# Optimization experiments

Hardware: AMD Instinct MI355X
Metric: run time of the kernel (lower is better)

## Reference

```python
import jax, jax.numpy as jnp
import numpy as np

N_NODES = 100000
N_EDGES = 400000
N_GRAPHS = 5000
F_IN = 64
H = 128
OUT = 1
N_LAYERS = 3  # gat_conv + 2 atom_gats
NEG_SLOPE = 0.01


def _gat_conv(x_src, x_dst, src, dst, W, a_src, a_dst, b, num_dst):
    """PyG GATConv, heads=1, add_self_loops=False, negative_slope=0.01.

    x_src: [Ns, Fin], x_dst: [Nd, Fin]; src/dst: [E] int; W: [Fin, H];
    a_src, a_dst, b: [H]. Returns [Nd, H].
    """
    hs = x_src @ W                      # [Ns, H]
    hd = x_dst @ W                      # [Nd, H]
    as_n = hs @ a_src                   # [Ns]
    ad_n = hd @ a_dst                   # [Nd]
    e = jax.nn.leaky_relu(as_n[src] + ad_n[dst], NEG_SLOPE)  # [E]
    # segment softmax over destination nodes
    seg_max = jax.ops.segment_max(e, dst, num_segments=num_dst)
    seg_max = jnp.where(jnp.isfinite(seg_max), seg_max, 0.0)
    ex = jnp.exp(e - seg_max[dst])
    denom = jax.ops.segment_sum(ex, dst, num_segments=num_dst) + 1e-16
    alpha = ex / denom[dst]             # [E]
    out = jax.ops.segment_sum(alpha[:, None] * hs[src], dst, num_segments=num_dst)
    return out + b


def setup_inputs() -> dict:
    key = jax.random.key(0)
    ks = jax.random.split(key, 16)
    x = jax.random.normal(ks[0], (N_NODES, F_IN), dtype=jnp.float32)
    edge_index = jax.random.randint(ks[1], (2, N_EDGES), 0, N_NODES, dtype=jnp.int64)
    batch = jnp.sort(jax.random.randint(ks[2], (N_NODES,), 0, N_GRAPHS, dtype=jnp.int64))
    s_in = 1.0 / np.sqrt(F_IN)
    s_h = 1.0 / np.sqrt(H)
    W1 = jax.random.uniform(ks[3], (F_IN, H), jnp.float32, -s_in, s_in)
    b1 = jax.random.uniform(ks[4], (H,), jnp.float32, -s_in, s_in)
    gW = jax.random.normal(ks[5], (N_LAYERS, H, H), jnp.float32) * s_h
    g_asrc = jax.random.normal(ks[6], (N_LAYERS, H), jnp.float32) * s_h
    g_adst = jax.random.normal(ks[7], (N_LAYERS, H), jnp.float32) * s_h
    g_b = jnp.zeros((N_LAYERS, H), jnp.float32)
    mW = jax.random.normal(ks[8], (H, H), jnp.float32) * s_h
    m_asrc = jax.random.normal(ks[9], (H,), jnp.float32) * s_h
    m_adst = jax.random.normal(ks[10], (H,), jnp.float32) * s_h
    m_b = jnp.zeros((H,), jnp.float32)
    W2 = jax.random.uniform(ks[11], (H, OUT), jnp.float32, -s_h, s_h)
    b2 = jax.random.uniform(ks[12], (OUT,), jnp.float32, -s_h, s_h)
    return {"x": x, "edge_index": edge_index, "batch": batch,
            "W1": W1, "b1": b1, "gW": gW, "g_asrc": g_asrc,
            "g_adst": g_adst, "g_b": g_b, "mW": mW, "m_asrc": m_asrc,
            "m_adst": m_adst, "m_b": m_b, "W2": W2, "b2": b2}


def reference(x, edge_index, batch, W1, b1, gW, g_asrc, g_adst, g_b,
              mW, m_asrc, m_adst, m_b, W2, b2):
    src, dst = edge_index[0], edge_index[1]
    h = jax.nn.leaky_relu(x @ W1 + b1, NEG_SLOPE)            # lin1 + leaky_relu_
    for i in range(N_LAYERS):                                 # gat_conv + atom_gats
        h = jax.nn.elu(_gat_conv(h, h, src, dst, gW[i], g_asrc[i],
                                 g_adst[i], g_b[i], N_NODES))
    # global readout: node -> graph bipartite GAT
    pooled = jax.nn.relu(jax.ops.segment_sum(h, batch, num_segments=N_GRAPHS))
    row = jnp.arange(N_NODES)
    out = jax.nn.elu(_gat_conv(h, pooled, row, batch, mW, m_asrc,
                               m_adst, m_b, N_GRAPHS))
    return out @ W2 + b2                                      # [N_GRAPHS, OUT]
```

## Files before the change

### kernel.cpp

```cpp
#include <hip/hip_runtime.h>
#include <hip/hip_fp16.h>
#include <math.h>
#include <stdint.h>

#define DEV __device__ __forceinline__

using f32x4 = __attribute__((ext_vector_type(4))) float;
using half8 = __attribute__((ext_vector_type(8))) _Float16;
typedef union { uint4 u; half8 h; } u4h8;

DEV float lrelu(float x){ return x > 0.f ? x : 0.01f*x; }
DEV float elu1(float x){ return x > 0.f ? x : __expf(x)-1.f; }

DEV int lower_bound_i(const int* __restrict__ a, int n, int key){
  int lo = 0, hi = n;
  while (lo < hi){ int mid = (lo+hi)>>1; if (a[mid] < key) lo = mid+1; else hi = mid; }
  return lo;
}

__global__ void wprep(const float* __restrict__ W, unsigned short* __restrict__ Hi,
                      unsigned short* __restrict__ Lo, int K, int tot){
  int idx = blockIdx.x*256 + threadIdx.x;
  if (idx >= tot) return;
  int kn = K*128;
  int mat = idx / kn;
  int rem = idx - mat*kn;
  int k = rem >> 7;
  int n = rem & 127;
  float v = W[idx];
  __half h = __float2half_rn(v);
  float lo = (v - __half2float(h)) * 1024.f;
  size_t o = (size_t)mat*kn + (size_t)n*K + k;
  Hi[o] = __half_as_ushort(h);
  Lo[o] = __half_as_ushort(__float2half_rn(lo));
}

__global__ __launch_bounds__(256, 3) void gemm_lin1(
    const float* __restrict__ X, const unsigned short* __restrict__ Wt_hi,
    const unsigned short* __restrict__ Wt_lo, const float* __restrict__ bias,
    unsigned short* __restrict__ Ch, int M)
{
  const int tid = threadIdx.x;
  const int lane = tid & 63;
  const int wv = tid >> 6;
  const int ml = lane & 15;
  const int kg = lane >> 4;
  const int R0 = blockIdx.x * 64;

  __shared__ uint32_t sA[2][1024];
  __shared__ float sC[4][32][36];

  const unsigned short* bhp[2];
  const unsigned short* blp[2];
  #pragma unroll
  for (int nt = 0; nt < 2; ++nt){
    int n = wv*32 + nt*16 + ml;
    bhp[nt] = Wt_hi + (size_t)n*64 + kg*8;
    blp[nt] = Wt_lo + (size_t)n*64 + kg*8;
  }

  {
    int row = tid >> 2, kq = tid & 3;
    int gr = R0 + row; gr = gr < M ? gr : M-1;
    const float4* xp = (const float4*)(X + (size_t)gr*64 + kq*16);
    int sub = kq >> 1;
    #pragma unroll
    for (int i = 0; i < 4; ++i){
      float4 v = xp[i];
      __half2 h0 = __floats2half2_rn(v.x, v.y);
      __half2 h1 = __floats2half2_rn(v.z, v.w);
      int slot = (kq & 1)*2 + (i >> 1);
      int slot_s = slot ^ ((row >> 1) & 3);
      int byte = row*64 + slot_s*16 + (i & 1)*8;
      *(uint2*)((char*)&sA[sub][0] + byte) = make_uint2(*(uint32_t*)&h0, *(uint32_t*)&h1);
    }
  }
  __syncthreads();

  f32x4 accH[4][2], accL[4][2];
  #pragma unroll
  for (int mt = 0; mt < 4; ++mt)
    #pragma unroll
    for (int nt = 0; nt < 2; ++nt){
      accH[mt][nt] = (f32x4){0.f,0.f,0.f,0.f};
      accL[mt][nt] = (f32x4){0.f,0.f,0.f,0.f};
    }

  #pragma unroll
  for (int sc = 0; sc < 2; ++sc){
    u4h8 bh[2], bl[2];
    #pragma unroll
    for (int nt = 0; nt < 2; ++nt){
      bh[nt].u = *(const uint4*)(bhp[nt] + sc*32);
      bl[nt].u = *(const uint4*)(blp[nt] + sc*32);
    }
    const char* buf = (const char*)&sA[sc][0];
    #pragma unroll
    for (int mt = 0; mt < 4; ++mt){
      int row = mt*16 + ml;
      int ba = row*64 + ((kg ^ ((row >> 1) & 3)) * 16);
      u4h8 A_;
      A_.u = *(const uint4*)(buf + ba);
      #pragma unroll
      for (int nt = 0; nt < 2; ++nt){
        accH[mt][nt] = __builtin_amdgcn_mfma_f32_16x16x32_f16(A_.h, bh[nt].h, accH[mt][nt], 0, 0, 0);
        accL[mt][nt] = __builtin_amdgcn_mfma_f32_16x16x32_f16(A_.h, bl[nt].h, accL[mt][nt], 0, 0, 0);
      }
    }
  }

  float bv[2] = { bias[wv*32 + ml], bias[wv*32 + 16 + ml] };
  #pragma unroll
  for (int p = 0; p < 2; ++p){
    #pragma unroll
    for (int mh = 0; mh < 2; ++mh){
      int mt = p*2 + mh;
      #pragma unroll
      for (int nt = 0; nt < 2; ++nt){
        #pragma unroll
        for (int r = 0; r < 4; ++r){
          float v = accH[mt][nt][r] + accL[mt][nt][r] * 9.765625e-4f;
          v = lrelu(v + bv[nt]);
          sC[wv][mh*16 + kg*4 + r][nt*16 + ml] = v;
        }
      }
    }
    __syncthreads();
    #pragma unroll
    for (int j = 0; j < 4; ++j){
      int row_l = j*8 + (lane >> 3);
      int c4 = (lane & 7) * 4;
      int grow = R0 + p*32 + row_l;
      if (grow < M){
        float4 v = *(const float4*)&sC[wv][row_l][c4];
        int gcol = wv*32 + c4;
        __half2 h0 = __floats2half2_rn(v.x, v.y);
        __half2 h1 = __floats2half2_rn(v.z, v.w);
        *(uint2*)(Ch + (size_t)grow*128 + gcol) = make_uint2(*(uint32_t*)&h0, *(uint32_t*)&h1);
      }
    }
    __syncthreads();
  }
}

template<int OUTMODE, bool DOTA, bool DOTB>
__global__ __launch_bounds__(256, 3) void gemm_mfma(
    const unsigned short* __restrict__ Ah, const unsigned short* __restrict__ Wt_hi,
    const unsigned short* __restrict__ Wt_lo,
    const float* __restrict__ va, const float* __restrict__ vb,
    unsigned short* __restrict__ Ch,
    float* __restrict__ outa, float* __restrict__ outb, int M)
{
  constexpr int K = 128;
  const int tid = threadIdx.x;
  const int lane = tid & 63;
  const int wv = tid >> 6;
  const int ml = lane & 15;
  const int kg = lane >> 4;
  const int R0 = blockIdx.x * 64;

  __shared__ uint32_t sA[4][1024];
  __shared__ float sC[4][32][36];
  __shared__ float sd[4][64][2];

  const unsigned short* bhp[2];
  const unsigned short* blp[2];
  #pragma unroll
  for (int nt = 0; nt < 2; ++nt){
    int n = wv*32 + nt*16 + ml;
    bhp[nt] = Wt_hi + (size_t)n*K + kg*8;
    blp[nt] = Wt_lo + (size_t)n*K + kg*8;
  }

  auto STAGE = [&](int ch){
    #pragma unroll
    for (int j = 0; j < 2; ++j){
      int sc = ch*2 + j;
      int o = tid*16;
      int row = o >> 6;
      int t = (o >> 4) & 3;
      int gr = R0 + row; gr = gr < M ? gr : M-1;
      int jj = t ^ ((row >> 1) & 3);
      const char* src = (const char*)(Ah + (size_t)gr*K + sc*32 + jj*8);
      char* dst = (char*)(&sA[(ch & 1)*2 + j][0]) + wv*1024;
      __builtin_amdgcn_global_load_lds(
          (const __attribute__((address_space(1))) void*)src,
          (__attribute__((address_space(3))) void*)dst, 16, 0, 0);
    }
  };

  f32x4 accH[4][2], accL[4][2];
  #pragma unroll
  for (int mt = 0; mt < 4; ++mt)
    #pragma unroll
    for (int nt = 0; nt < 2; ++nt){
      accH[mt][nt] = (f32x4){0.f,0.f,0.f,0.f};
      accL[mt][nt] = (f32x4){0.f,0.f,0.f,0.f};
    }

  STAGE(0);
  u4h8 bh[2][2], bl[2][2];
  #pragma unroll
  for (int j = 0; j < 2; ++j)
    #pragma unroll
    for (int nt = 0; nt < 2; ++nt){
      bh[j][nt].u = *(const uint4*)(bhp[nt] + j*32);
      bl[j][nt].u = *(const uint4*)(blp[nt] + j*32);
    }
  __syncthreads();

  #pragma unroll
  for (int ch = 0; ch < 2; ++ch){
    u4h8 bhN[2][2], blN[2][2];
    if (ch == 0){
      STAGE(1);
      #pragma unroll
      for (int j = 0; j < 2; ++j)
        #pragma unroll
        for (int nt = 0; nt < 2; ++nt){
          bhN[j][nt].u = *(const uint4*)(bhp[nt] + (2 + j)*32);
          blN[j][nt].u = *(const uint4*)(blp[nt] + (2 + j)*32);
        }
    }
    #pragma unroll
    for (int js = 0; js < 2; ++js){
      const char* buf = (const char*)&sA[(ch & 1)*2 + js][0];
      #pragma unroll
      for (int mt = 0; mt < 4; ++mt){
        int row = mt*16 + ml;
        int ba = row*64 + ((kg ^ ((row >> 1) & 3)) * 16);
        u4h8 A_;
        A_.u = *(const uint4*)(buf + ba);
        #pragma unroll
        for (int nt = 0; nt < 2; ++nt){
          accH[mt][nt] = __builtin_amdgcn_mfma_f32_16x16x32_f16(A_.h, bh[js][nt].h, accH[mt][nt], 0, 0, 0);
          accL[mt][nt] = __builtin_amdgcn_mfma_f32_16x16x32_f16(A_.h, bl[js][nt].h, accL[mt][nt], 0, 0, 0);
        }
      }
    }
    __syncthreads();
    if (ch == 0){
      #pragma unroll
      for (int j = 0; j < 2; ++j)
        #pragma unroll
        for (int nt = 0; nt < 2; ++nt){ bh[j][nt] = bhN[j][nt]; bl[j][nt] = blN[j][nt]; }
    }
  }

  #pragma unroll
  for (int mt = 0; mt < 4; ++mt)
    #pragma unroll
    for (int nt = 0; nt < 2; ++nt)
      accH[mt][nt] = accH[mt][nt] + accL[mt][nt] * 9.765625e-4f;

  if constexpr (DOTA || DOTB){
    float vaL[2] = {0.f,0.f}, vbL[2] = {0.f,0.f};
    if constexpr (DOTA){ vaL[0] = va[wv*32 + ml]; vaL[1] = va[wv*32 + 16 + ml]; }
    if constexpr (DOTB){ vbL[0] = vb[wv*32 + ml]; vbL[1] = vb[wv*32 + 16 + ml]; }
    #pragma unroll
    for (int mt = 0; mt < 4; ++mt){
      #pragma unroll
      for (int r = 0; r < 4; ++r){
        float pa = 0.f, pb = 0.f;
        #pragma unroll
        for (int nt = 0; nt < 2; ++nt){
          float v = accH[mt][nt][r];
          if constexpr (DOTA) pa = fmaf(v, vaL[nt], pa);
          if constexpr (DOTB) pb = fmaf(v, vbL[nt], pb);
        }
        #pragma unroll
        for (int o = 8; o; o >>= 1){
          if constexpr (DOTA) pa += __shfl_xor(pa, o, 64);
          if constexpr (DOTB) pb += __shfl_xor(pb, o, 64);
        }
        if (ml == 0){
          int rl = mt*16 + kg*4 + r;
          sd[wv][rl][0] = pa;
          sd[wv][rl][1] = pb;
        }
      }
    }
    __syncthreads();
    if (tid < 64){
      int row = R0 + tid;
      if (row < M){
        if constexpr (DOTA)
          outa[row] = sd[0][tid][0] + sd[1][tid][0] + sd[2][tid][0] + sd[3][tid][0];
        if constexpr (DOTB)
          outb[row] = sd[0][tid][1] + sd[1][tid][1] + sd[2][tid][1] + sd[3][tid][1];
      }
    }
  }

  if constexpr (OUTMODE == 2){
    if constexpr (DOTA || DOTB) __syncthreads();
    #pragma unroll
    for (int p = 0; p < 2; ++p){
      #pragma unroll
      for (int mh = 0; mh < 2; ++mh){
        int mt = p*2 + mh;
        #pragma unroll
        for (int nt = 0; nt < 2; ++nt){
          #pragma unroll
          for (int r = 0; r < 4; ++r)
            sC[wv][mh*16 + kg*4 + r][nt*16 + ml] = accH[mt][nt][r];
        }
      }
      __syncthreads();
      #pragma unroll
      for (int j = 0; j < 4; ++j){
        int row_l = j*8 + (lane >> 3);
        int c4 = (lane & 7) * 4;
        int grow = R0 + p*32 + row_l;
        if (grow < M){
          float4 v = *(const float4*)&sC[wv][row_l][c4];
          int gcol = wv*32 + c4;
          __half2 h0 = __floats2half2_rn(v.x, v.y);
          __half2 h1 = __floats2half2_rn(v.z, v.w);
          *(uint2*)(Ch + (size_t)grow*128 + gcol) = make_uint2(*(uint32_t*)&h0, *(uint32_t*)&h1);
        }
      }
      __syncthreads();
    }
  }
}

__global__ void hist_k(const int* __restrict__ dstv, int* __restrict__ deg, int E){
  int e = blockIdx.x*256 + threadIdx.x;
  if (e < E) atomicAdd(&deg[dstv[e]], 1);
}

__global__ void scan_sum(const int* __restrict__ deg, int* __restrict__ bsum, int n){
  __shared__ int s4[4];
  int i = blockIdx.x*256 + threadIdx.x;
  int v = (i < n) ? deg[i] : 0;
  #pragma unroll
  for (int o = 32; o; o >>= 1) v += __shfl_down(v, o, 64);
  if ((threadIdx.x & 63) == 0) s4[threadIdx.x >> 6] = v;
  __syncthreads();
  if (threadIdx.x == 0) bsum[blockIdx.x] = s4[0]+s4[1]+s4[2]+s4[3];
}

__global__ void scan_blocksums(int* __restrict__ bsum, int nb){
  __shared__ int s[512];
  int t = threadIdx.x;
  s[t] = (t < nb) ? bsum[t] : 0;
  __syncthreads();
  for (int o = 1; o < 512; o <<= 1){
    int v = s[t];
    int u = (t >= o) ? s[t-o] : 0;
    __syncthreads();
    s[t] = v + u;
    __syncthreads();
  }
  if (t < nb) bsum[t] = t ? s[t-1] : 0;
}

__global__ void scan_final(const int* __restrict__ deg, const int* __restrict__ boff,
    int* __restrict__ rp, int* __restrict__ cur, int n, int E)
{
  __shared__ int wsum[4];
  int i = blockIdx.x*256 + threadIdx.x;
  int lane = threadIdx.x & 63, wv = threadIdx.x >> 6;
  int v = (i < n) ? deg[i] : 0;
  int inc = v;
  #pragma unroll
  for (int o = 1; o < 64; o <<= 1){
    int u = __shfl_up(inc, o, 64);
    if (lane >= o) inc += u;
  }
  if (lane == 63) wsum[wv] = inc;
  __syncthreads();
  int woff = boff[blockIdx.x];
  for (int wq = 0; wq < wv; ++wq) woff += wsum[wq];
  int excl = woff + inc - v;
  if (i < n){ rp[i] = excl; cur[i] = excl; }
  if (blockIdx.x == 0 && threadIdx.x == 0) rp[n] = E;
}

__global__ void scatter_k(const int* __restrict__ srcv, const int* __restrict__ dstv,
                          int* __restrict__ cur, int* __restrict__ ssorted, int E){
  int e = blockIdx.x*256 + threadIdx.x;
  if (e < E){
    int p = atomicAdd(&cur[dstv[e]], 1);
    ssorted[p] = srcv[e];
  }
}

DEV void gstep(const __half2* __restrict__ hs16, int lane, float alpha, int sid, int i,
               float& a0, float& a1){
  float al = __uint_as_float(__builtin_amdgcn_readlane(__float_as_uint(alpha), i));
  int sd = __builtin_amdgcn_readlane(sid, i);
  float2 f = __half22float2(hs16[(size_t)sd*64 + lane]);
  a0 = fmaf(al, f.x, a0);
  a1 = fmaf(al, f.y, a1);
}

__global__ __launch_bounds__(256) void gat_agg(const int* __restrict__ ssorted,
    const int* __restrict__ rp,
    const float* __restrict__ asn, const float* __restrict__ adn,
    const __half2* __restrict__ hs16, const float* __restrict__ bias,
    __half2* __restrict__ outp, int Nn)
{
  const int lane = threadIdx.x & 63;
  const int wv = threadIdx.x >> 6;
  const int d = blockIdx.x*4 + wv;
  if (d >= Nn) return;
  const int lo = rp[d], hi = rp[d+1];
  const int deg = hi - lo;
  float acc0 = 0.f, acc1 = 0.f;
  if (deg > 0){
    const float ad = adn[d];
    if (deg <= 64){
      int sid = 0; float lg = -1e30f;
      if (lane < deg){
        sid = ssorted[lo + lane];
        lg = lrelu(asn[sid] + ad);
      }
      float m = lg;
      if (deg <= 8){
        if (deg > 4) m = fmaxf(m, __shfl_xor(m, 4, 64));
        m = fmaxf(m, __shfl_xor(m, 2, 64));
        m = fmaxf(m, __shfl_xor(m, 1, 64));
        float p = (lane < deg) ? __expf(lg - m) : 0.f;
        float s = p;
        if (deg > 4) s += __shfl_xor(s, 4, 64);
        s += __shfl_xor(s, 2, 64);
        s += __shfl_xor(s, 1, 64);
        float alpha = p * (1.f / (s + 1e-16f));
        gstep(hs16, lane, alpha, sid, 0, acc0, acc1);
        gstep(hs16, lane, alpha, sid, 1, acc0, acc1);
        gstep(hs16, lane, alpha, sid, 2, acc0, acc1);
        gstep(hs16, lane, alpha, sid, 3, acc0, acc1);
        if (deg > 4){
          gstep(hs16, lane, alpha, sid, 4, acc0, acc1);
          gstep(hs16, lane, alpha, sid, 5, acc0, acc1);
          gstep(hs16, lane, alpha, sid, 6, acc0, acc1);
          gstep(hs16, lane, alpha, sid, 7, acc0, acc1);
        }
      } else {
        #pragma unroll
        for (int o = 32; o; o >>= 1) m = fmaxf(m, __shfl_xor(m, o, 64));
        float p = (lane < deg) ? __expf(lg - m) : 0.f;
        float s = p;
        #pragma unroll
        for (int o = 32; o; o >>= 1) s += __shfl_xor(s, o, 64);
        float alpha = p * (1.f / (s + 1e-16f));
        for (int base = 0; base < deg; base += 8){
          #pragma unroll
          for (int i = 0; i < 8; ++i)
            gstep(hs16, lane, alpha, sid, base + i, acc0, acc1);
        }
      }
    } else {
      float m = -1e30f;
      for (int e = lane; e < deg; e += 64){
        int sid = ssorted[lo+e];
        m = fmaxf(m, lrelu(asn[sid] + ad));
      }
      #pragma unroll
      for (int o = 32; o; o >>= 1) m = fmaxf(m, __shfl_xor(m, o, 64));
      float s = 0.f;
      for (int e = lane; e < deg; e += 64){
        int sid = ssorted[lo+e];
        s += __expf(lrelu(asn[sid] + ad) - m);
      }
      #pragma unroll
      for (int o = 32; o; o >>= 1) s += __shfl_xor(s, o, 64);
      float inv = 1.f / (s + 1e-16f);
      for (int e = 0; e < deg; ++e){
        int sid = ssorted[lo+e];
        float a = __expf(lrelu(asn[sid] + ad) - m) * inv;
        float2 f = __half22float2(hs16[(size_t)sid*64 + lane]);
        acc0 = fmaf(a, f.x, acc0);
        acc1 = fmaf(a, f.y, acc1);
      }
    }
  }
  float2 bb = *(const float2*)(bias + lane*2);
  outp[(size_t)d*64 + lane] = __floats2half2_rn(elu1(acc0 + bb.x), elu1(acc1 + bb.y));
}

__global__ __launch_bounds__(128) void pool_relu(const unsigned short* __restrict__ h16,
    const int* __restrict__ batch, unsigned short* __restrict__ ptail, int Nn)
{
  const int g = blockIdx.x;
  const int c = threadIdx.x;
  __shared__ int sb[2];
  if (c < 2) sb[c] = lower_bound_i(batch, Nn, g + c);
  __syncthreads();
  const int lo = sb[0], hi = sb[1];
  float s = 0.f;
  for (int i = lo; i < hi; ++i)
    s += __half2float(__ushort_as_half(h16[(size_t)i*128 + c]));
  ptail[(size_t)g*128 + c] = __half_as_ushort(__float2half_rn(fmaxf(s, 0.f)));
}

__global__ __launch_bounds__(128) void mol_agg(const float* __restrict__ as2,
    const float* __restrict__ ad2, const unsigned short* __restrict__ hs2,
    const int* __restrict__ batch, const float* __restrict__ bias,
    const float* __restrict__ W2, const float* __restrict__ b2,
    float* __restrict__ out, int Nn)
{
  const int g = blockIdx.x;
  const int c = threadIdx.x;
  __shared__ int sb[2];
  __shared__ float red[2];
  if (c < 2) sb[c] = lower_bound_i(batch, Nn, g + c);
  __syncthreads();
  const int lo = sb[0], hi = sb[1];
  const float ad = ad2[g];

  float mt = -1e30f;
  for (int i = lo + c; i < hi; i += 128) mt = fmaxf(mt, lrelu(as2[i] + ad));
  #pragma unroll
  for (int o = 32; o; o >>= 1) mt = fmaxf(mt, __shfl_xor(mt, o, 64));
  if ((c & 63) == 0) red[c >> 6] = mt;
  __syncthreads();
  const float m = fmaxf(red[0], red[1]);

  float st = 0.f;
  for (int i = lo + c; i < hi; i += 128) st += __expf(lrelu(as2[i] + ad) - m);
  #pragma unroll
  for (int o = 32; o; o >>= 1) st += __shfl_xor(st, o, 64);
  __syncthreads();
  if ((c & 63) == 0) red[c >> 6] = st;
  __syncthreads();
  const float inv = 1.f / (red[0] + red[1] + 1e-16f);

  float acc = 0.f;
  for (int i = lo; i < hi; ++i){
    float wgt = __expf(lrelu(as2[i] + ad) - m) * inv;
    acc = fmaf(wgt, __half2float(__ushort_as_half(hs2[(size_t)i*128 + c])), acc);
  }
  float v = elu1(acc + bias[c]);

  float r = v * W2[c];
  #pragma unroll
  for (int o = 32; o; o >>= 1) r += __shfl_xor(r, o, 64);
  __syncthreads();
  if ((c & 63) == 0) red[c >> 6] = r;
  __syncthreads();
  if (c == 0) out[g] = red[0] + red[1] + b2[0];
}

extern "C" void kernel_launch(void* const* d_in, const int* in_sizes, int n_in,
                              void* d_out, int out_size, void* d_ws, size_t ws_size,
                              hipStream_t stream)
{
  const float* x      = (const float*)d_in[0];
  const int*   ei     = (const int*)  d_in[1];
  const int*   batch  = (const int*)  d_in[2];
  const float* W1     = (const float*)d_in[3];
  const float* b1     = (const float*)d_in[4];
  const float* gW     = (const float*)d_in[5];
  const float* g_asrc = (const float*)d_in[6];
  const float* g_adst = (const float*)d_in[7];
  const float* g_b    = (const float*)d_in[8];
  const float* mW     = (const float*)d_in[9];
  const float* m_asrc = (const float*)d_in[10];
  const float* m_adst = (const float*)d_in[11];
  const float* m_b    = (const float*)d_in[12];
  const float* W2     = (const float*)d_in[13];
  const float* b2     = (const float*)d_in[14];

  const int Nn = in_sizes[0] / 64;
  const int E  = in_sizes[1] / 2;
  const int G  = out_size;
  const int NL = in_sizes[5] / (128*128);
  const int M2 = Nn + G;
  const int* srcv = ei;
  const int* dstv = ei + E;

  char* w = (char*)d_ws;
  unsigned short* h16 = (unsigned short*)w; w += (size_t)(M2+64)*128*2;
  unsigned short* hsR = (unsigned short*)w; w += (size_t)(M2+64)*128*2;
  float* asO      = (float*)w; w += (size_t)(M2+64)*4;
  float* adO      = (float*)w; w += (size_t)(M2+64)*4;
  int*   deg      = (int*)w;   w += (size_t)Nn*4;
  int*   rp       = (int*)w;   w += (size_t)(Nn+64)*4;
  int*   cur      = (int*)w;   w += (size_t)Nn*4;
  int*   ssorted  = (int*)w;   w += (size_t)E*4;
  int*   bsum     = (int*)w;   w += 4096;
  unsigned short* w1h = (unsigned short*)w; w += 64*128*2;
  unsigned short* w1l = (unsigned short*)w; w += 64*128*2;
  unsigned short* gwh = (unsigned short*)w; w += (size_t)NL*128*128*2;
  unsigned short* gwl = (unsigned short*)w; w += (size_t)NL*128*128*2;
  unsigned short* mwh = (unsigned short*)w; w += 128*128*2;
  unsigned short* mwl = (unsigned short*)w; w += 128*128*2;

  const int nscan = (Nn + 255)/256;
  const int nrt = (Nn + 63)/64;
  const int mrt = (M2 + 63)/64;

  hipMemsetAsync(deg, 0, (size_t)Nn*4, stream);
  hist_k<<<(E+255)/256, 256, 0, stream>>>(dstv, deg, E);
  scan_sum<<<nscan, 256, 0, stream>>>(deg, bsum, Nn);
  scan_blocksums<<<1, 512, 0, stream>>>(bsum, nscan);
  scan_final<<<nscan, 256, 0, stream>>>(deg, bsum, rp, cur, Nn, E);
  scatter_k<<<(E+255)/256, 256, 0, stream>>>(srcv, dstv, cur, ssorted, E);

  wprep<<<((64*128)+255)/256, 256, 0, stream>>>(W1, w1h, w1l, 64, 64*128);
  wprep<<<((NL*128*128)+255)/256, 256, 0, stream>>>(gW, gwh, gwl, 128, NL*128*128);
  wprep<<<((128*128)+255)/256, 256, 0, stream>>>(mW, mwh, mwl, 128, 128*128);

  gemm_lin1<<<nrt, 256, 0, stream>>>(x, w1h, w1l, b1, h16, Nn);

  for (int l = 0; l < NL; ++l){
    gemm_mfma<2, true, true><<<nrt, 256, 0, stream>>>(
        h16, gwh + (size_t)l*128*128, gwl + (size_t)l*128*128,
        g_asrc + l*128, g_adst + l*128, hsR, asO, adO, Nn);
    gat_agg<<<(Nn+3)/4, 256, 0, stream>>>(ssorted, rp, asO, adO,
        (const __half2*)hsR, g_b + l*128, (__half2*)h16, Nn);
  }

  pool_relu<<<G, 128, 0, stream>>>(h16, batch, h16 + (size_t)Nn*128, Nn);
  gemm_mfma<2, true, true><<<mrt, 256, 0, stream>>>(
      h16, mwh, mwl, m_asrc, m_adst, hsR, asO, adO, M2);
  mol_agg<<<G, 128, 0, stream>>>(asO, adO + Nn, hsR, batch, m_b, W2, b2, (float*)d_out, Nn);
}
```

Baseline: 347.7 us.

## Pack four nodes per wavefront in GAT aggregation, fuse prep and scan kernels

```diff
diff --git a/kernel.cpp b/kernel.cpp
--- a/kernel.cpp
+++ b/kernel.cpp
@@ -18,21 +18,38 @@
   return lo;
 }
 
-__global__ void wprep(const float* __restrict__ W, unsigned short* __restrict__ Hi,
-                      unsigned short* __restrict__ Lo, int K, int tot){
-  int idx = blockIdx.x*256 + threadIdx.x;
-  if (idx >= tot) return;
-  int kn = K*128;
-  int mat = idx / kn;
-  int rem = idx - mat*kn;
-  int k = rem >> 7;
-  int n = rem & 127;
-  float v = W[idx];
+DEV void wsplit(float v, unsigned short* __restrict__ H, unsigned short* __restrict__ L, size_t o){
   __half h = __float2half_rn(v);
   float lo = (v - __half2float(h)) * 1024.f;
-  size_t o = (size_t)mat*kn + (size_t)n*K + k;
-  Hi[o] = __half_as_ushort(h);
-  Lo[o] = __half_as_ushort(__float2half_rn(lo));
+  H[o] = __half_as_ushort(h);
+  L[o] = __half_as_ushort(__float2half_rn(lo));
+}
+
+__global__ void wprep_all(const float* __restrict__ W1, const float* __restrict__ gW,
+    const float* __restrict__ mW,
+    unsigned short* __restrict__ w1h, unsigned short* __restrict__ w1l,
+    unsigned short* __restrict__ gwh, unsigned short* __restrict__ gwl,
+    unsigned short* __restrict__ mwh, unsigned short* __restrict__ mwl,
+    int* __restrict__ deg, unsigned long long* __restrict__ bstat,
+    int* __restrict__ bctr, int Nn, int nG, int nscan)
+{
+  int i = blockIdx.x*256 + threadIdx.x;
+  if (i < Nn) deg[i] = 0;
+  if (i < nscan) bstat[i] = 0ull;
+  if (i == 0) *bctr = 0;
+  if (i < 8192){
+    int k = i >> 7, n = i & 127;
+    wsplit(W1[i], w1h, w1l, (size_t)n*64 + k);
+  }
+  if (i < nG){
+    int mat = i >> 14; int rem = i & 16383;
+    int k = rem >> 7, n = rem & 127;
+    wsplit(gW[i], gwh, gwl, (size_t)mat*16384 + (size_t)n*128 + k);
+  }
+  if (i < 16384){
+    int k = i >> 7, n = i & 127;
+    wsplit(mW[i], mwh, mwl, (size_t)n*128 + k);
+  }
 }
 
 __global__ __launch_bounds__(256, 3) void gemm_lin1(
@@ -330,37 +347,17 @@
   if (e < E) atomicAdd(&deg[dstv[e]], 1);
 }
 
-__global__ void scan_sum(const int* __restrict__ deg, int* __restrict__ bsum, int n){
-  __shared__ int s4[4];
-  int i = blockIdx.x*256 + threadIdx.x;
-  int v = (i < n) ? deg[i] : 0;
-  #pragma unroll
-  for (int o = 32; o; o >>= 1) v += __shfl_down(v, o, 64);
-  if ((threadIdx.x & 63) == 0) s4[threadIdx.x >> 6] = v;
-  __syncthreads();
-  if (threadIdx.x == 0) bsum[blockIdx.x] = s4[0]+s4[1]+s4[2]+s4[3];
-}
-
-__global__ void scan_blocksums(int* __restrict__ bsum, int nb){
-  __shared__ int s[512];
-  int t = threadIdx.x;
-  s[t] = (t < nb) ? bsum[t] : 0;
-  __syncthreads();
-  for (int o = 1; o < 512; o <<= 1){
-    int v = s[t];
-    int u = (t >= o) ? s[t-o] : 0;
-    __syncthreads();
-    s[t] = v + u;
-    __syncthreads();
-  }
-  if (t < nb) bsum[t] = t ? s[t-1] : 0;
-}
-
-__global__ void scan_final(const int* __restrict__ deg, const int* __restrict__ boff,
-    int* __restrict__ rp, int* __restrict__ cur, int n, int E)
-{
-  __shared__ int wsum[4];
-  int i = blockIdx.x*256 + threadIdx.x;
+__global__ void scan_onepass(const int* __restrict__ deg, int* __restrict__ rp,
+    int* __restrict__ cur, unsigned long long* __restrict__ bstat,
+    int* __restrict__ bctr, int n, int E)
+{
+  __shared__ int sbid;
+  __shared__ int swsum[4];
+  __shared__ int sprev;
+  if (threadIdx.x == 0) sbid = atomicAdd(bctr, 1);
+  __syncthreads();
+  const int bid = sbid;
+  int i = bid*256 + threadIdx.x;
   int lane = threadIdx.x & 63, wv = threadIdx.x >> 6;
   int v = (i < n) ? deg[i] : 0;
   int inc = v;
@@ -369,13 +366,27 @@
     int u = __shfl_up(inc, o, 64);
     if (lane >= o) inc += u;
   }
-  if (lane == 63) wsum[wv] = inc;
-  __syncthreads();
-  int woff = boff[blockIdx.x];
-  for (int wq = 0; wq < wv; ++wq) woff += wsum[wq];
+  if (lane == 63) swsum[wv] = inc;
+  __syncthreads();
+  if (threadIdx.x == 0){
+    int bsum = swsum[0]+swsum[1]+swsum[2]+swsum[3];
+    atomicExch(&bstat[bid], (1ull << 62) | (unsigned long long)(unsigned)bsum);
+    int prev = 0;
+    for (int j = bid - 1; j >= 0; --j){
+      unsigned long long s;
+      do { s = atomicAdd(&bstat[j], 0ull); } while ((s >> 62) == 0);
+      prev += (int)(s & 0xffffffffull);
+      if ((s >> 62) == 2) break;
+    }
+    atomicExch(&bstat[bid], (2ull << 62) | (unsigned long long)(unsigned)(prev + bsum));
+    sprev = prev;
+  }
+  __syncthreads();
+  int woff = sprev;
+  for (int wq = 0; wq < wv; ++wq) woff += swsum[wq];
   int excl = woff + inc - v;
   if (i < n){ rp[i] = excl; cur[i] = excl; }
-  if (blockIdx.x == 0 && threadIdx.x == 0) rp[n] = E;
+  if (bid == 0 && threadIdx.x == 0) rp[n] = E;
 }
 
 __global__ void scatter_k(const int* __restrict__ srcv, const int* __restrict__ dstv,
@@ -387,113 +398,137 @@
   }
 }
 
-DEV void gstep(const __half2* __restrict__ hs16, int lane, float alpha, int sid, int i,
-               float& a0, float& a1){
-  float al = __uint_as_float(__builtin_amdgcn_readlane(__float_as_uint(alpha), i));
-  int sd = __builtin_amdgcn_readlane(sid, i);
-  float2 f = __half22float2(hs16[(size_t)sd*64 + lane]);
-  a0 = fmaf(al, f.x, a0);
-  a1 = fmaf(al, f.y, a1);
-}
-
 __global__ __launch_bounds__(256) void gat_agg(const int* __restrict__ ssorted,
     const int* __restrict__ rp,
     const float* __restrict__ asn, const float* __restrict__ adn,
-    const __half2* __restrict__ hs16, const float* __restrict__ bias,
-    __half2* __restrict__ outp, int Nn)
+    const uint4* __restrict__ hsv, const float* __restrict__ bias,
+    uint4* __restrict__ outv, int Nn)
 {
   const int lane = threadIdx.x & 63;
   const int wv = threadIdx.x >> 6;
-  const int d = blockIdx.x*4 + wv;
-  if (d >= Nn) return;
-  const int lo = rp[d], hi = rp[d+1];
-  const int deg = hi - lo;
-  float acc0 = 0.f, acc1 = 0.f;
-  if (deg > 0){
-    const float ad = adn[d];
-    if (deg <= 64){
-      int sid = 0; float lg = -1e30f;
-      if (lane < deg){
-        sid = ssorted[lo + lane];
-        lg = lrelu(asn[sid] + ad);
-      }
-      float m = lg;
-      if (deg <= 8){
-        if (deg > 4) m = fmaxf(m, __shfl_xor(m, 4, 64));
-        m = fmaxf(m, __shfl_xor(m, 2, 64));
-        m = fmaxf(m, __shfl_xor(m, 1, 64));
-        float p = (lane < deg) ? __expf(lg - m) : 0.f;
-        float s = p;
-        if (deg > 4) s += __shfl_xor(s, 4, 64);
-        s += __shfl_xor(s, 2, 64);
-        s += __shfl_xor(s, 1, 64);
-        float alpha = p * (1.f / (s + 1e-16f));
-        gstep(hs16, lane, alpha, sid, 0, acc0, acc1);
-        gstep(hs16, lane, alpha, sid, 1, acc0, acc1);
-        gstep(hs16, lane, alpha, sid, 2, acc0, acc1);
-        gstep(hs16, lane, alpha, sid, 3, acc0, acc1);
-        if (deg > 4){
-          gstep(hs16, lane, alpha, sid, 4, acc0, acc1);
-          gstep(hs16, lane, alpha, sid, 5, acc0, acc1);
-          gstep(hs16, lane, alpha, sid, 6, acc0, acc1);
-          gstep(hs16, lane, alpha, sid, 7, acc0, acc1);
-        }
-      } else {
-        #pragma unroll
-        for (int o = 32; o; o >>= 1) m = fmaxf(m, __shfl_xor(m, o, 64));
-        float p = (lane < deg) ? __expf(lg - m) : 0.f;
-        float s = p;
-        #pragma unroll
-        for (int o = 32; o; o >>= 1) s += __shfl_xor(s, o, 64);
-        float alpha = p * (1.f / (s + 1e-16f));
-        for (int base = 0; base < deg; base += 8){
-          #pragma unroll
-          for (int i = 0; i < 8; ++i)
-            gstep(hs16, lane, alpha, sid, base + i, acc0, acc1);
-        }
-      }
-    } else {
-      float m = -1e30f;
-      for (int e = lane; e < deg; e += 64){
-        int sid = ssorted[lo+e];
-        m = fmaxf(m, lrelu(asn[sid] + ad));
-      }
-      #pragma unroll
-      for (int o = 32; o; o >>= 1) m = fmaxf(m, __shfl_xor(m, o, 64));
-      float s = 0.f;
-      for (int e = lane; e < deg; e += 64){
-        int sid = ssorted[lo+e];
-        s += __expf(lrelu(asn[sid] + ad) - m);
-      }
-      #pragma unroll
-      for (int o = 32; o; o >>= 1) s += __shfl_xor(s, o, 64);
-      float inv = 1.f / (s + 1e-16f);
-      for (int e = 0; e < deg; ++e){
-        int sid = ssorted[lo+e];
-        float a = __expf(lrelu(asn[sid] + ad) - m) * inv;
-        float2 f = __half22float2(hs16[(size_t)sid*64 + lane]);
-        acc0 = fmaf(a, f.x, acc0);
-        acc1 = fmaf(a, f.y, acc1);
-      }
-    }
-  }
-  float2 bb = *(const float2*)(bias + lane*2);
-  outp[(size_t)d*64 + lane] = __floats2half2_rn(elu1(acc0 + bb.x), elu1(acc1 + bb.y));
-}
-
-__global__ __launch_bounds__(128) void pool_relu(const unsigned short* __restrict__ h16,
-    const int* __restrict__ batch, unsigned short* __restrict__ ptail, int Nn)
-{
-  const int g = blockIdx.x;
-  const int c = threadIdx.x;
-  __shared__ int sb[2];
-  if (c < 2) sb[c] = lower_bound_i(batch, Nn, g + c);
-  __syncthreads();
-  const int lo = sb[0], hi = sb[1];
-  float s = 0.f;
-  for (int i = lo; i < hi; ++i)
-    s += __half2float(__ushort_as_half(h16[(size_t)i*128 + c]));
-  ptail[(size_t)g*128 + c] = __half_as_ushort(__float2half_rn(fmaxf(s, 0.f)));
+  const int l16 = lane & 15;
+  const int gbase = lane & 48;
+  const int d = blockIdx.x*16 + wv*4 + (lane >> 4);
+  const bool valid = d < Nn;
+  const int dc = valid ? d : Nn-1;
+  const int lo = rp[dc], hi = rp[dc+1];
+  const int deg = valid ? (hi - lo) : 0;
+  const float ad = adn[dc];
+  float acc[8] = {0.f,0.f,0.f,0.f,0.f,0.f,0.f,0.f};
+
+  const bool fast = (deg <= 16);
+  const int fdeg = fast ? deg : 0;
+  int mdeg = fdeg;
+  mdeg = max(mdeg, __shfl_xor(mdeg, 16, 64));
+  mdeg = max(mdeg, __shfl_xor(mdeg, 32, 64));
+
+  int sid = 0; float lg = -1e30f;
+  if (l16 < fdeg){
+    sid = ssorted[lo + l16];
+    lg = lrelu(asn[sid] + ad);
+  }
+  float m = lg;
+  m = fmaxf(m, __shfl_xor(m, 8, 64));
+  m = fmaxf(m, __shfl_xor(m, 4, 64));
+  m = fmaxf(m, __shfl_xor(m, 2, 64));
+  m = fmaxf(m, __shfl_xor(m, 1, 64));
+  float p = (l16 < fdeg) ? __expf(lg - m) : 0.f;
+  float s = p;
+  s += __shfl_xor(s, 8, 64);
+  s += __shfl_xor(s, 4, 64);
+  s += __shfl_xor(s, 2, 64);
+  s += __shfl_xor(s, 1, 64);
+  float alpha = p * (1.f / (s + 1e-16f));
+
+  for (int i = 0; i < mdeg; ++i){
+    if (i < fdeg){
+      float al = __shfl(alpha, gbase + i, 64);
+      int sd = __shfl(sid, gbase + i, 64);
+      uint4 v = hsv[(size_t)sd*16 + l16];
+      float2 f0 = __half22float2(*(__half2*)&v.x);
+      float2 f1 = __half22float2(*(__half2*)&v.y);
+      float2 f2 = __half22float2(*(__half2*)&v.z);
+      float2 f3 = __half22float2(*(__half2*)&v.w);
+      acc[0] = fmaf(al, f0.x, acc[0]); acc[1] = fmaf(al, f0.y, acc[1]);
+      acc[2] = fmaf(al, f1.x, acc[2]); acc[3] = fmaf(al, f1.y, acc[3]);
+      acc[4] = fmaf(al, f2.x, acc[4]); acc[5] = fmaf(al, f2.y, acc[5]);
+      acc[6] = fmaf(al, f3.x, acc[6]); acc[7] = fmaf(al, f3.y, acc[7]);
+    }
+  }
+
+  if (!fast){
+    float mg = -1e30f;
+    for (int e = l16; e < deg; e += 16){
+      int sd = ssorted[lo + e];
+      mg = fmaxf(mg, lrelu(asn[sd] + ad));
+    }
+    mg = fmaxf(mg, __shfl_xor(mg, 8, 64));
+    mg = fmaxf(mg, __shfl_xor(mg, 4, 64));
+    mg = fmaxf(mg, __shfl_xor(mg, 2, 64));
+    mg = fmaxf(mg, __shfl_xor(mg, 1, 64));
+    float sg = 0.f;
+    for (int e = l16; e < deg; e += 16){
+      int sd = ssorted[lo + e];
+      sg += __expf(lrelu(asn[sd] + ad) - mg);
+    }
+    sg += __shfl_xor(sg, 8, 64);
+    sg += __shfl_xor(sg, 4, 64);
+    sg += __shfl_xor(sg, 2, 64);
+    sg += __shfl_xor(sg, 1, 64);
+    float inv = 1.f / (sg + 1e-16f);
+    for (int e = 0; e < deg; ++e){
+      int sd = ssorted[lo + e];
+      float a = __expf(lrelu(asn[sd] + ad) - mg) * inv;
+      uint4 v = hsv[(size_t)sd*16 + l16];
+      float2 f0 = __half22float2(*(__half2*)&v.x);
+      float2 f1 = __half22float2(*(__half2*)&v.y);
+      float2 f2 = __half22float2(*(__half2*)&v.z);
+      float2 f3 = __half22float2(*(__half2*)&v.w);
+      acc[0] = fmaf(a, f0.x, acc[0]); acc[1] = fmaf(a, f0.y, acc[1]);
+      acc[2] = fmaf(a, f1.x, acc[2]); acc[3] = fmaf(a, f1.y, acc[3]);
+      acc[4] = fmaf(a, f2.x, acc[4]); acc[5] = fmaf(a, f2.y, acc[5]);
+      acc[6] = fmaf(a, f3.x, acc[6]); acc[7] = fmaf(a, f3.y, acc[7]);
+    }
+  }
+
+  if (valid){
+    float4 b0 = ((const float4*)bias)[l16*2];
+    float4 b1 = ((const float4*)bias)[l16*2 + 1];
+    __half2 h0 = __floats2half2_rn(elu1(acc[0]+b0.x), elu1(acc[1]+b0.y));
+    __half2 h1 = __floats2half2_rn(elu1(acc[2]+b0.z), elu1(acc[3]+b0.w));
+    __half2 h2 = __floats2half2_rn(elu1(acc[4]+b1.x), elu1(acc[5]+b1.y));
+    __half2 h3 = __floats2half2_rn(elu1(acc[6]+b1.z), elu1(acc[7]+b1.w));
+    outv[(size_t)d*16 + l16] = make_uint4(*(uint32_t*)&h0, *(uint32_t*)&h1,
+                                          *(uint32_t*)&h2, *(uint32_t*)&h3);
+  }
+}
+
+__global__ __launch_bounds__(256) void pool_relu(const uint4* __restrict__ hv,
+    const int* __restrict__ batch, uint4* __restrict__ ptail, int Nn, int G)
+{
+  const int lane = threadIdx.x & 63;
+  const int wv = threadIdx.x >> 6;
+  const int l16 = lane & 15;
+  const int g = blockIdx.x*16 + wv*4 + (lane >> 4);
+  if (g >= G) return;
+  const int lo = lower_bound_i(batch, Nn, g);
+  const int hi = lower_bound_i(batch, Nn, g + 1);
+  float acc[8] = {0.f,0.f,0.f,0.f,0.f,0.f,0.f,0.f};
+  for (int i = lo; i < hi; ++i){
+    uint4 v = hv[(size_t)i*16 + l16];
+    float2 f0 = __half22float2(*(__half2*)&v.x);
+    float2 f1 = __half22float2(*(__half2*)&v.y);
+    float2 f2 = __half22float2(*(__half2*)&v.z);
+    float2 f3 = __half22float2(*(__half2*)&v.w);
+    acc[0] += f0.x; acc[1] += f0.y; acc[2] += f1.x; acc[3] += f1.y;
+    acc[4] += f2.x; acc[5] += f2.y; acc[6] += f3.x; acc[7] += f3.y;
+  }
+  __half2 h0 = __floats2half2_rn(fmaxf(acc[0],0.f), fmaxf(acc[1],0.f));
+  __half2 h1 = __floats2half2_rn(fmaxf(acc[2],0.f), fmaxf(acc[3],0.f));
+  __half2 h2 = __floats2half2_rn(fmaxf(acc[4],0.f), fmaxf(acc[5],0.f));
+  __half2 h3 = __floats2half2_rn(fmaxf(acc[6],0.f), fmaxf(acc[7],0.f));
+  ptail[(size_t)g*16 + l16] = make_uint4(*(uint32_t*)&h0, *(uint32_t*)&h1,
+                                         *(uint32_t*)&h2, *(uint32_t*)&h3);
 }
 
 __global__ __launch_bounds__(128) void mol_agg(const float* __restrict__ as2,
@@ -581,7 +616,8 @@
   int*   rp       = (int*)w;   w += (size_t)(Nn+64)*4;
   int*   cur      = (int*)w;   w += (size_t)Nn*4;
   int*   ssorted  = (int*)w;   w += (size_t)E*4;
-  int*   bsum     = (int*)w;   w += 4096;
+  unsigned long long* bstat = (unsigned long long*)w; w += 512*8;
+  int*   bctr     = (int*)w;   w += 64;
   unsigned short* w1h = (unsigned short*)w; w += 64*128*2;
   unsigned short* w1l = (unsigned short*)w; w += 64*128*2;
   unsigned short* gwh = (unsigned short*)w; w += (size_t)NL*128*128*2;
@@ -593,16 +629,12 @@
   const int nrt = (Nn + 63)/64;
   const int mrt = (M2 + 63)/64;
 
-  hipMemsetAsync(deg, 0, (size_t)Nn*4, stream);
+  wprep_all<<<nscan, 256, 0, stream>>>(W1, gW, mW, w1h, w1l, gwh, gwl, mwh, mwl,
+                                       deg, bstat, bctr, Nn, NL*16384, nscan);
+
   hist_k<<<(E+255)/256, 256, 0, stream>>>(dstv, deg, E);
-  scan_sum<<<nscan, 256, 0, stream>>>(deg, bsum, Nn);
-  scan_blocksums<<<1, 512, 0, stream>>>(bsum, nscan);
-  scan_final<<<nscan, 256, 0, stream>>>(deg, bsum, rp, cur, Nn, E);
+  scan_onepass<<<nscan, 256, 0, stream>>>(deg, rp, cur, bstat, bctr, Nn, E);
   scatter_k<<<(E+255)/256, 256, 0, stream>>>(srcv, dstv, cur, ssorted, E);
-
-  wprep<<<((64*128)+255)/256, 256, 0, stream>>>(W1, w1h, w1l, 64, 64*128);
-  wprep<<<((NL*128*128)+255)/256, 256, 0, stream>>>(gW, gwh, gwl, 128, NL*128*128);
-  wprep<<<((128*128)+255)/256, 256, 0, stream>>>(mW, mwh, mwl, 128, 128*128);
 
   gemm_lin1<<<nrt, 256, 0, stream>>>(x, w1h, w1l, b1, h16, Nn);
 
@@ -610,11 +642,12 @@
     gemm_mfma<2, true, true><<<nrt, 256, 0, stream>>>(
         h16, gwh + (size_t)l*128*128, gwl + (size_t)l*128*128,
         g_asrc + l*128, g_adst + l*128, hsR, asO, adO, Nn);
-    gat_agg<<<(Nn+3)/4, 256, 0, stream>>>(ssorted, rp, asO, adO,
-        (const __half2*)hsR, g_b + l*128, (__half2*)h16, Nn);
-  }
-
-  pool_relu<<<G, 128, 0, stream>>>(h16, batch, h16 + (size_t)Nn*128, Nn);
+    gat_agg<<<(Nn+15)/16, 256, 0, stream>>>(ssorted, rp, asO, adO,
+        (const uint4*)hsR, g_b + l*128, (uint4*)h16, Nn);
+  }
+
+  pool_relu<<<(G+15)/16, 256, 0, stream>>>((const uint4*)h16, batch,
+      (uint4*)(h16 + (size_t)Nn*128), Nn, G);
   gemm_mfma<2, true, true><<<mrt, 256, 0, stream>>>(
       h16, mwh, mwl, m_asrc, m_adst, hsR, asO, adO, M2);
   mol_agg<<<G, 128, 0, stream>>>(asO, adO + Nn, hsR, batch, m_b, W2, b2, (float*)d_out, Nn);
```

New measurement: 318.1 us. 1.09x faster.
